# Kernel tuning notes

Hardware: AMD Instinct MI355X
Metric: run time of the kernel (lower is better)

The kernel has to match this reference:

```python
import jax, jax.numpy as jnp
import numpy as np

N = 100000
E = 1600000
DIN = 165
DH = 128


def setup_inputs() -> dict:
    key = jax.random.key(0)
    ks = jax.random.split(key, 10)
    def nrm(k, shape, scale=0.1):
        return jax.random.normal(k, shape, dtype=jnp.float32) * scale
    x = jax.random.normal(ks[0], (N, DIN), dtype=jnp.float32)
    edge_index = jax.random.randint(ks[1], (2, E), 0, N, dtype=jnp.int64)
    return dict(
        x=x,
        edge_index=edge_index,
        fb_w1=nrm(ks[2], (DIN, DIN // 2)),
        fb_w2=nrm(ks[3], (DIN // 2, DIN)),
        sage_wl=nrm(ks[4], (DIN, DH)),
        sage_bl=jnp.zeros((DH,), jnp.float32),
        sage_wr=nrm(ks[5], (DIN, DH)),
        gat_w=nrm(ks[6], (DH, DH // 2)),
        gat_att_src=nrm(ks[7], (DH // 2,)),
        gat_att_dst=nrm(ks[8], (DH // 2,)),
        gat_b=jnp.zeros((DH // 2,), jnp.float32),
        cheb_w=nrm(ks[9], (DH // 2, 1)),
        cheb_b=jnp.zeros((1,), jnp.float32),
    )


def _segment_softmax(logits, seg, num_segments):
    mx = jax.ops.segment_max(logits, seg, num_segments=num_segments)
    e = jnp.exp(logits - mx[seg])
    s = jax.ops.segment_sum(e, seg, num_segments=num_segments)
    return e / (s[seg] + 1e-16)


def reference(x, edge_index, fb_w1, fb_w2, sage_wl, sage_bl, sage_wr,
              gat_w, gat_att_src, gat_att_dst, gat_b, cheb_w, cheb_b):
    n = x.shape[0]
    src, dst = edge_index[0], edge_index[1]

    # FeatureBooster: scatter over batch=arange(n) is identity for max and sum,
    # so max_result == sum_result == x and y = sigmoid(mlp(x) + mlp(x)).
    m = jnp.maximum(x @ fb_w1, 0.0) @ fb_w2
    x = x * jax.nn.sigmoid(m + m)

    # SAGEConv (mean aggregation): out = lin_l(mean_agg(x_src -> dst)) + lin_r(x)
    agg = jax.ops.segment_sum(x[src], dst, num_segments=n)  # [n, DIN]
    cnt = jax.ops.segment_sum(jnp.ones((src.shape[0],), x.dtype), dst, num_segments=n)
    agg = agg / jnp.maximum(cnt, 1.0)[:, None]
    x = agg @ sage_wl + sage_bl + x @ sage_wr
    x = jnp.maximum(x, 0.0)  # relu; dropout is identity in eval mode

    # GATConv (heads=1) with default add_self_loops=True
    ar = jnp.arange(n, dtype=src.dtype)
    si = jnp.concatenate([src, ar])
    di = jnp.concatenate([dst, ar])
    h = x @ gat_w                      # [n, 64]
    a_s = h @ gat_att_src              # [n]
    a_d = h @ gat_att_dst              # [n]
    e = a_s[si] + a_d[di]
    e = jnp.where(e > 0, e, 0.2 * e)   # leaky_relu slope 0.2
    alpha = _segment_softmax(e, di, n)
    x = jax.ops.segment_sum(h[si] * alpha[:, None], di, num_segments=n) + gat_b
    x = jnp.maximum(x, 0.0)

    # ChebConv with K=1: T_0(x) = x, so it's a plain linear layer.
    x = x @ cheb_w + cheb_b
    return jax.nn.sigmoid(x)
```

## Files before the change

kernel.cpp:

```cpp
#include <hip/hip_runtime.h>
#include <hip/hip_bf16.h>

#define N_NODES 100000
#define N_EDGES 1600000
#define EQ 400000
#define DIN 165
#define DHID 82
#define DH 128
#define DG 64
#define XPS 168
#define HS 88
#define SLOTS 60
#define SCB 96

typedef _Float16 f16;
typedef f16 f16x8 __attribute__((ext_vector_type(8)));
typedef f16 f16x4 __attribute__((ext_vector_type(4)));
typedef float f32x4 __attribute__((ext_vector_type(4)));

#define MFMA16(a, b, c) __builtin_amdgcn_mfma_f32_16x16x32_f16(a, b, c, 0, 0, 0)


__device__ __forceinline__ void scatter_edges(int e0, int e1, int tg,
                                              const int* __restrict__ dst,
                                              const int* __restrict__ src,
                                              int* __restrict__ cnt,
                                              int* __restrict__ slots) {
    for (int e = e0 + tg; e < e1; e += SCB * 256) {
        int d = dst[e];
        int r = atomicAdd(&cnt[d], 1);
        if (r < SLOTS) slots[(long)d * SLOTS + r] = src[e];
    }
}

__global__ __launch_bounds__(256) void xpad_kernel(const float* __restrict__ x,
                                                   f16* __restrict__ Xp,
                                                   const int* __restrict__ dst,
                                                   const int* __restrict__ src,
                                                   int* __restrict__ cnt,
                                                   int* __restrict__ slots) {
    if (blockIdx.x < SCB) {
        scatter_edges(0, EQ, blockIdx.x * 256 + threadIdx.x, dst, src, cnt, slots);
        return;
    }
    int gid = (blockIdx.x - SCB) * 256 + threadIdx.x;
    if (gid >= N_NODES * 42) return;
    int node = gid / 42, g = gid % 42;
    int col0 = g * 4;
    f16x4 o;
#pragma unroll
    for (int j = 0; j < 4; j++) {
        int c = col0 + j;
        o[j] = (f16)((c < DIN) ? x[(long)node * DIN + c] : 0.f);
    }
    *((f16x4*)(Xp + (long)node * XPS + col0)) = o;
}

__global__ __launch_bounds__(256) void h_fill_kernel(const f16* __restrict__ Xp,
                                                     const float* __restrict__ w1,
                                                     f16* __restrict__ H,
                                                     const int* __restrict__ dst,
                                                     const int* __restrict__ src,
                                                     int* __restrict__ cnt,
                                                     int* __restrict__ slots) {
    int tid = threadIdx.x, wave = tid >> 6, lane = tid & 63;
    if (blockIdx.x < SCB) {
        scatter_edges(EQ, 2 * EQ, blockIdx.x * 256 + tid, dst, src, cnt, slots);
        return;
    }
    int q = lane >> 4, l16 = lane & 15;
    int blk = blockIdx.x - SCB;
    int g = (blk >> 3) & 1;
    int chunk = (blk & 7) + 8 * (blk >> 4);
    int nbase = g * 48;
    f16x8 bf[3][6];
#pragma unroll
    for (int nt = 0; nt < 3; nt++) {
        int col = nbase + nt * 16 + l16;
#pragma unroll
        for (int ks = 0; ks < 6; ks++) {
            int kb = ks * 32 + q * 8;
            f16x8 b;
#pragma unroll
            for (int j = 0; j < 8; j++) {
                int k = kb + j;
                b[j] = (f16)((k < DIN && col < DHID) ? w1[k * DHID + col] : 0.f);
            }
            bf[nt][ks] = b;
        }
    }
    for (int mt = chunk * 4 + wave; mt < 6250; mt += 768) {
        const f16* xr = Xp + (long)(mt * 16 + l16) * XPS;
        f32x4 acc[3];
#pragma unroll
        for (int nt = 0; nt < 3; nt++) acc[nt] = (f32x4){0.f, 0.f, 0.f, 0.f};
#pragma unroll
        for (int ks = 0; ks < 6; ks++) {
            f16x8 a = *((const f16x8*)(xr + ks * 32 + q * 8));
#pragma unroll
            for (int nt = 0; nt < 3; nt++) acc[nt] = MFMA16(a, bf[nt][ks], acc[nt]);
        }
#pragma unroll
        for (int nt = 0; nt < 3; nt++) {
            int col = nbase + nt * 16 + l16;
            if (col < HS) {
#pragma unroll
                for (int r = 0; r < 4; r++) {
                    int node = mt * 16 + q * 4 + r;
                    H[(long)node * HS + col] = (f16)fmaxf(acc[nt][r], 0.f);
                }
            }
        }
    }
}

__global__ __launch_bounds__(256) void y_kernel(const f16* __restrict__ Xp,
                                                const f16* __restrict__ H,
                                                const float* __restrict__ w2,
                                                f16* __restrict__ Y,
                                                const int* __restrict__ dst,
                                                const int* __restrict__ src,
                                                int* __restrict__ cnt,
                                                int* __restrict__ slots) {
    int tid = threadIdx.x, wave = tid >> 6, lane = tid & 63;
    if (blockIdx.x < SCB) {
        scatter_edges(2 * EQ, 3 * EQ, blockIdx.x * 256 + tid, dst, src, cnt, slots);
        return;
    }
    int q = lane >> 4, l16 = lane & 15;
    int blk = blockIdx.x - SCB;
    int g = (blk >> 3) & 3;
    int chunk = (blk & 7) + 8 * (blk >> 5);
    int nbase = g * 48;
    f16x8 bf[3][3];
#pragma unroll
    for (int nt = 0; nt < 3; nt++) {
        int col = nbase + nt * 16 + l16;
#pragma unroll
        for (int ks = 0; ks < 3; ks++) {
            int kb = ks * 32 + q * 8;
            f16x8 b;
#pragma unroll
            for (int j = 0; j < 8; j++) {
                int k = kb + j;
                b[j] = (f16)((k < DHID && col < DIN) ? w2[k * DIN + col] : 0.f);
            }
            bf[nt][ks] = b;
        }
    }
    for (int mt = chunk * 4 + wave; mt < 6250; mt += 768) {
        const f16* hr = H + (long)(mt * 16 + l16) * HS;
        f32x4 acc[3];
#pragma unroll
        for (int nt = 0; nt < 3; nt++) acc[nt] = (f32x4){0.f, 0.f, 0.f, 0.f};
#pragma unroll
        for (int ks = 0; ks < 3; ks++) {
            f16x8 a = *((const f16x8*)(hr + ks * 32 + q * 8));
#pragma unroll
            for (int nt = 0; nt < 3; nt++) acc[nt] = MFMA16(a, bf[nt][ks], acc[nt]);
        }
#pragma unroll
        for (int nt = 0; nt < 3; nt++) {
            int col = nbase + nt * 16 + l16;
            if (col < XPS) {
#pragma unroll
                for (int r = 0; r < 4; r++) {
                    int node = mt * 16 + q * 4 + r;
                    float gg = 1.f / (1.f + __expf(-2.f * acc[nt][r]));
                    float xv = (float)Xp[(long)node * XPS + col];
                    Y[(long)node * XPS + col] = (f16)(xv * gg);
                }
            }
        }
    }
}

__global__ __launch_bounds__(256) void sage_lin_kernel(const f16* __restrict__ Y,
                                                       const float* __restrict__ wl,
                                                       const float* __restrict__ wr,
                                                       const float* __restrict__ bl,
                                                       f16* __restrict__ t_l,
                                                       f16* __restrict__ x2,
                                                       const int* __restrict__ dst,
                                                       const int* __restrict__ src,
                                                       int* __restrict__ cnt,
                                                       int* __restrict__ slots) {
    int tid = threadIdx.x, wave = tid >> 6, lane = tid & 63;
    if (blockIdx.x < SCB) {
        scatter_edges(3 * EQ, N_EDGES, blockIdx.x * 256 + tid, dst, src, cnt, slots);
        return;
    }
    int q = lane >> 4, l16 = lane & 15;
    int blk = blockIdx.x - SCB;
    int g = (blk >> 3) & 3;
    int chunk = (blk & 7) + 8 * (blk >> 5);
    bool isR = (g >= 2);
    const float* W = isR ? wr : wl;
    int cbase = (g & 1) * 64;
    f16x8 bf[4][6];
    float blv[4];
#pragma unroll
    for (int nt = 0; nt < 4; nt++) {
        int col = cbase + nt * 16 + l16;
        blv[nt] = isR ? bl[col] : 0.f;
#pragma unroll
        for (int ks = 0; ks < 6; ks++) {
            int kb = ks * 32 + q * 8;
            f16x8 b;
#pragma unroll
            for (int j = 0; j < 8; j++) {
                int k = kb + j;
                b[j] = (f16)((k < DIN) ? W[k * DH + col] : 0.f);
            }
            bf[nt][ks] = b;
        }
    }
    for (int mt = chunk * 4 + wave; mt < 6250; mt += 768) {
        const f16* yrow = Y + (long)(mt * 16 + l16) * XPS;
        f32x4 acc[4];
#pragma unroll
        for (int nt = 0; nt < 4; nt++) acc[nt] = (f32x4){0.f, 0.f, 0.f, 0.f};
#pragma unroll
        for (int ks = 0; ks < 6; ks++) {
            f16x8 a = *((const f16x8*)(yrow + ks * 32 + q * 8));
#pragma unroll
            for (int nt = 0; nt < 4; nt++) acc[nt] = MFMA16(a, bf[nt][ks], acc[nt]);
        }
#pragma unroll
        for (int nt = 0; nt < 4; nt++) {
            int col = cbase + nt * 16 + l16;
#pragma unroll
            for (int r = 0; r < 4; r++) {
                int node = mt * 16 + q * 4 + r;
                if (isR)
                    x2[(long)node * DH + col] = (f16)(acc[nt][r] + blv[nt]);
                else
                    t_l[(long)node * DH + col] = (f16)acc[nt][r];
            }
        }
    }
}

__global__ __launch_bounds__(256) void sage_agg_kernel(const f16* __restrict__ t_l,
                                                       const int* __restrict__ cnt,
                                                       const int* __restrict__ slots,
                                                       f16* __restrict__ x2) {
    int wid = threadIdx.x >> 6, lane = threadIdx.x & 63;
    int i = blockIdx.x * 4 + wid;
    int deg = cnt[i];
    int quarter = lane >> 4, fq = lane & 15;
    float acc[8];
#pragma unroll
    for (int k = 0; k < 8; k++) acc[k] = 0.f;
    int sn_v = (lane < deg) ? slots[(long)i * SLOTS + lane] : 0;
    int jmax = (deg + 3) >> 2;
    for (int j = 0; j < jmax; j++) {
        int idx = 4 * j + quarter;
        int sn = __shfl(sn_v, idx);
        float v = (idx < deg) ? 1.f : 0.f;
        f16x8 p = *((const f16x8*)(t_l + ((long)sn << 7) + fq * 8));
#pragma unroll
        for (int k = 0; k < 8; k++) acc[k] = fmaf(v, (float)p[k], acc[k]);
    }
#pragma unroll
    for (int k = 0; k < 8; k++) {
        acc[k] += __shfl_xor(acc[k], 16);
        acc[k] += __shfl_xor(acc[k], 32);
    }
    if (quarter == 0) {
        float inv = 1.f / fmaxf((float)deg, 1.f);
        f16x8* xp = (f16x8*)(x2 + (long)i * DH + fq * 8);
        f16x8 pre = *xp;
        f16x8 o;
#pragma unroll
        for (int k = 0; k < 8; k++) o[k] = (f16)fmaxf((float)pre[k] + acc[k] * inv, 0.f);
        *xp = o;
    }
}

__global__ __launch_bounds__(256) void gat_h_kernel(const f16* __restrict__ x2,
                                                    const float* __restrict__ gw,
                                                    const float* __restrict__ att_s_w,
                                                    const float* __restrict__ att_d_w,
                                                    f16* __restrict__ h,
                                                    float* __restrict__ a_s,
                                                    float* __restrict__ a_d) {
    int tid = threadIdx.x, wave = tid >> 6, lane = tid & 63;
    int q = lane >> 4, l16 = lane & 15;
    f16x8 bf[4][4];
    float asw[4], adw[4];
#pragma unroll
    for (int nt = 0; nt < 4; nt++) {
        int col = nt * 16 + l16;
        asw[nt] = att_s_w[col];
        adw[nt] = att_d_w[col];
#pragma unroll
        for (int ks = 0; ks < 4; ks++) {
            int kb = ks * 32 + q * 8;
            f16x8 b;
#pragma unroll
            for (int j = 0; j < 8; j++) b[j] = (f16)gw[(kb + j) * DG + col];
            bf[nt][ks] = b;
        }
    }
    int stride = gridDim.x * 4;
    for (int mt = blockIdx.x * 4 + wave; mt < 6250; mt += stride) {
        const f16* xr = x2 + (long)(mt * 16 + l16) * DH;
        f32x4 acc[4];
#pragma unroll
        for (int nt = 0; nt < 4; nt++) acc[nt] = (f32x4){0.f, 0.f, 0.f, 0.f};
#pragma unroll
        for (int ks = 0; ks < 4; ks++) {
            f16x8 a = *((const f16x8*)(xr + ks * 32 + q * 8));
#pragma unroll
            for (int nt = 0; nt < 4; nt++) acc[nt] = MFMA16(a, bf[nt][ks], acc[nt]);
        }
#pragma unroll
        for (int r = 0; r < 4; r++) {
            int node = mt * 16 + q * 4 + r;
            float vs = 0.f, vd = 0.f;
#pragma unroll
            for (int nt = 0; nt < 4; nt++) {
                float hv = acc[nt][r];
                h[(long)node * DG + nt * 16 + l16] = (f16)hv;
                vs += hv * asw[nt];
                vd += hv * adw[nt];
            }
#pragma unroll
            for (int off = 1; off < 16; off <<= 1) {
                vs += __shfl_xor(vs, off);
                vd += __shfl_xor(vd, off);
            }
            if (l16 == 0) {
                a_s[node] = vs;
                a_d[node] = vd;
            }
        }
    }
}

__device__ __forceinline__ float leaky02(float v) { return v > 0.f ? v : 0.2f * v; }

__global__ __launch_bounds__(256) void gat_agg_kernel(const f16* __restrict__ h,
                                                      const float* __restrict__ a_s,
                                                      const float* __restrict__ a_d,
                                                      const int* __restrict__ cnt,
                                                      const int* __restrict__ slots,
                                                      const float* __restrict__ gat_b,
                                                      const float* __restrict__ cheb_w,
                                                      const float* __restrict__ cheb_b,
                                                      float* __restrict__ out) {
    int wid = threadIdx.x >> 6, lane = threadIdx.x & 63;
    int i = blockIdx.x * 4 + wid;
    int deg = cnt[i];
    int quarter = lane >> 4, fq = lane & 15;
    float adi = a_d[i];
    float acc[4] = {0.f, 0.f, 0.f, 0.f};
    int sn_v = (lane < deg) ? slots[(long)i * SLOTS + lane] : 0;
    float ev = 0.f;
    if (lane < deg) ev = __expf(leaky02(a_s[sn_v] + adi));
    float sv = ev;
    int jmax = (deg + 3) >> 2;
    for (int j = 0; j < jmax; j++) {
        int idx = 4 * j + quarter;
        int sn = __shfl(sn_v, idx);
        float w = __shfl(ev, idx);
        f16x4 p = *((const f16x4*)(h + ((long)sn << 6) + fq * 4));
#pragma unroll
        for (int k = 0; k < 4; k++) acc[k] = fmaf(w, (float)p[k], acc[k]);
    }
#pragma unroll
    for (int off = 32; off > 0; off >>= 1) sv += __shfl_xor(sv, off);
#pragma unroll
    for (int k = 0; k < 4; k++) {
        acc[k] += __shfl_xor(acc[k], 16);
        acc[k] += __shfl_xor(acc[k], 32);
    }
    if (quarter == 0) {
        float wself = __expf(leaky02(a_s[i] + adi));
        float s = sv + wself;
        f16x4 ph = *((const f16x4*)(h + ((long)i << 6) + fq * 4));
        float4 gb = ((const float4*)gat_b)[fq];
        float4 cw = ((const float4*)cheb_w)[fq];
        float gbv[4] = {gb.x, gb.y, gb.z, gb.w};
        float cwv[4] = {cw.x, cw.y, cw.z, cw.w};
        float inv = 1.f / s;
        float z = 0.f;
#pragma unroll
        for (int k = 0; k < 4; k++) {
            float o = fmaxf(fmaf(wself, (float)ph[k], acc[k]) * inv + gbv[k], 0.f);
            z = fmaf(o, cwv[k], z);
        }
#pragma unroll
        for (int off = 8; off > 0; off >>= 1) z += __shfl_xor(z, off);
        if (fq == 0) out[i] = 1.f / (1.f + __expf(-(z + cheb_b[0])));
    }
}

extern "C" void kernel_launch(void* const* d_in, const int* in_sizes, int n_in,
                              void* d_out, int out_size, void* d_ws, size_t ws_size,
                              hipStream_t stream) {
    const float* x       = (const float*)d_in[0];
    const int*   eidx    = (const int*)d_in[1];
    const float* fb_w1   = (const float*)d_in[2];
    const float* fb_w2   = (const float*)d_in[3];
    const float* sage_wl = (const float*)d_in[4];
    const float* sage_bl = (const float*)d_in[5];
    const float* sage_wr = (const float*)d_in[6];
    const float* gat_w   = (const float*)d_in[7];
    const float* att_src = (const float*)d_in[8];
    const float* att_dst = (const float*)d_in[9];
    const float* gat_b   = (const float*)d_in[10];
    const float* cheb_w  = (const float*)d_in[11];
    const float* cheb_b  = (const float*)d_in[12];

    const int* src = eidx;
    const int* dst = eidx + N_EDGES;

    char* base = (char*)d_ws;
    f16* Xp  = (f16*)base;
    f16* H   = (f16*)(base + 33600000);
    f16* Y   = (f16*)(base + 51200000);
    f16* t_l = (f16*)base;
    f16* x2  = (f16*)(base + 25600000);
    f16* h   = (f16*)(base + 51200000);
    float* a_s = (float*)(base + 64000000);
    float* a_d = a_s + N_NODES;
    int* cnt   = (int*)(base + 84800000);
    int* slots = (int*)(base + 85200000);

    hipMemsetAsync(cnt, 0, N_NODES * sizeof(int), stream);

    xpad_kernel<<<SCB + (N_NODES * 42 + 255) / 256, 256, 0, stream>>>(
        x, Xp, dst, src, cnt, slots);
    h_fill_kernel<<<SCB + 384, 256, 0, stream>>>(Xp, fb_w1, H, dst, src, cnt, slots);
    y_kernel<<<SCB + 768, 256, 0, stream>>>(Xp, H, fb_w2, Y, dst, src, cnt, slots);
    sage_lin_kernel<<<SCB + 768, 256, 0, stream>>>(Y, sage_wl, sage_wr, sage_bl,
                                                   t_l, x2, dst, src, cnt, slots);
    sage_agg_kernel<<<N_NODES / 4, 256, 0, stream>>>(t_l, cnt, slots, x2);
    gat_h_kernel<<<392, 256, 0, stream>>>(x2, gat_w, att_src, att_dst, h, a_s, a_d);
    gat_agg_kernel<<<N_NODES / 4, 256, 0, stream>>>(h, a_s, a_d, cnt, slots, gat_b,
                                                    cheb_w, cheb_b, (float*)d_out);
}
```

Before: 456.3 us.

## Fuse SAGE mean aggregation with GAT linear projection via shared-memory tile

Merges the SAGE neighbor aggregation kernel and the GAT h/attention projection kernel into one. Each block aggregates 16 nodes into a shared-memory tile, then runs MFMA on that tile to produce h, a_s and a_d, so the post-ReLU x2 no longer makes a global write-and-reload round trip. It also adds one kernel fewer and clamps the degree to SLOTS. In exchange, each block must reload the GAT weights from global memory and wait at a barrier between the gather and the MFMA phase, which may reduce latency hiding during the gather.

```diff
diff --git a/kernel.cpp b/kernel.cpp
--- a/kernel.cpp
+++ b/kernel.cpp
@@ -12,6 +12,7 @@
 #define HS 88
 #define SLOTS 60
 #define SCB 96
+#define TLP 136
 
 typedef _Float16 f16;
 typedef f16 f16x8 __attribute__((ext_vector_type(8)));
@@ -241,101 +242,96 @@
     }
 }
 
-__global__ __launch_bounds__(256) void sage_agg_kernel(const f16* __restrict__ t_l,
-                                                       const int* __restrict__ cnt,
-                                                       const int* __restrict__ slots,
-                                                       f16* __restrict__ x2) {
-    int wid = threadIdx.x >> 6, lane = threadIdx.x & 63;
-    int i = blockIdx.x * 4 + wid;
-    int deg = cnt[i];
+__global__ __launch_bounds__(256) void sage_agg_gat_kernel(const f16* __restrict__ t_l,
+                                                           const f16* __restrict__ x2pre,
+                                                           const int* __restrict__ cnt,
+                                                           const int* __restrict__ slots,
+                                                           const float* __restrict__ gw,
+                                                           const float* __restrict__ att_s_w,
+                                                           const float* __restrict__ att_d_w,
+                                                           f16* __restrict__ h,
+                                                           float* __restrict__ a_s,
+                                                           float* __restrict__ a_d) {
+    __shared__ f16 tile[16 * TLP];
+    __shared__ float ps[4][16], pd[4][16];
+    int tid = threadIdx.x, wid = tid >> 6, lane = tid & 63;
     int quarter = lane >> 4, fq = lane & 15;
-    float acc[8];
-#pragma unroll
-    for (int k = 0; k < 8; k++) acc[k] = 0.f;
-    int sn_v = (lane < deg) ? slots[(long)i * SLOTS + lane] : 0;
-    int jmax = (deg + 3) >> 2;
-    for (int j = 0; j < jmax; j++) {
-        int idx = 4 * j + quarter;
-        int sn = __shfl(sn_v, idx);
-        float v = (idx < deg) ? 1.f : 0.f;
-        f16x8 p = *((const f16x8*)(t_l + ((long)sn << 7) + fq * 8));
-#pragma unroll
-        for (int k = 0; k < 8; k++) acc[k] = fmaf(v, (float)p[k], acc[k]);
-    }
-#pragma unroll
-    for (int k = 0; k < 8; k++) {
-        acc[k] += __shfl_xor(acc[k], 16);
-        acc[k] += __shfl_xor(acc[k], 32);
-    }
-    if (quarter == 0) {
-        float inv = 1.f / fmaxf((float)deg, 1.f);
-        f16x8* xp = (f16x8*)(x2 + (long)i * DH + fq * 8);
-        f16x8 pre = *xp;
-        f16x8 o;
-#pragma unroll
-        for (int k = 0; k < 8; k++) o[k] = (f16)fmaxf((float)pre[k] + acc[k] * inv, 0.f);
-        *xp = o;
-    }
-}
-
-__global__ __launch_bounds__(256) void gat_h_kernel(const f16* __restrict__ x2,
-                                                    const float* __restrict__ gw,
-                                                    const float* __restrict__ att_s_w,
-                                                    const float* __restrict__ att_d_w,
-                                                    f16* __restrict__ h,
-                                                    float* __restrict__ a_s,
-                                                    float* __restrict__ a_d) {
-    int tid = threadIdx.x, wave = tid >> 6, lane = tid & 63;
-    int q = lane >> 4, l16 = lane & 15;
-    f16x8 bf[4][4];
-    float asw[4], adw[4];
-#pragma unroll
-    for (int nt = 0; nt < 4; nt++) {
-        int col = nt * 16 + l16;
-        asw[nt] = att_s_w[col];
-        adw[nt] = att_d_w[col];
-#pragma unroll
-        for (int ks = 0; ks < 4; ks++) {
-            int kb = ks * 32 + q * 8;
-            f16x8 b;
-#pragma unroll
-            for (int j = 0; j < 8; j++) b[j] = (f16)gw[(kb + j) * DG + col];
-            bf[nt][ks] = b;
-        }
-    }
-    int stride = gridDim.x * 4;
-    for (int mt = blockIdx.x * 4 + wave; mt < 6250; mt += stride) {
-        const f16* xr = x2 + (long)(mt * 16 + l16) * DH;
-        f32x4 acc[4];
-#pragma unroll
-        for (int nt = 0; nt < 4; nt++) acc[nt] = (f32x4){0.f, 0.f, 0.f, 0.f};
-#pragma unroll
-        for (int ks = 0; ks < 4; ks++) {
-            f16x8 a = *((const f16x8*)(xr + ks * 32 + q * 8));
-#pragma unroll
-            for (int nt = 0; nt < 4; nt++) acc[nt] = MFMA16(a, bf[nt][ks], acc[nt]);
-        }
-#pragma unroll
-        for (int r = 0; r < 4; r++) {
-            int node = mt * 16 + q * 4 + r;
-            float vs = 0.f, vd = 0.f;
-#pragma unroll
-            for (int nt = 0; nt < 4; nt++) {
-                float hv = acc[nt][r];
-                h[(long)node * DG + nt * 16 + l16] = (f16)hv;
-                vs += hv * asw[nt];
-                vd += hv * adw[nt];
-            }
-#pragma unroll
-            for (int off = 1; off < 16; off <<= 1) {
-                vs += __shfl_xor(vs, off);
-                vd += __shfl_xor(vd, off);
-            }
-            if (l16 == 0) {
-                a_s[node] = vs;
-                a_d[node] = vd;
-            }
-        }
+    int base = blockIdx.x * 16;
+
+    int q = quarter, l16 = fq;
+    f16x8 bf[4];
+#pragma unroll
+    for (int ks = 0; ks < 4; ks++) {
+        int kb = ks * 32 + q * 8;
+        f16x8 b;
+#pragma unroll
+        for (int j = 0; j < 8; j++) b[j] = (f16)gw[(kb + j) * DG + wid * 16 + l16];
+        bf[ks] = b;
+    }
+    float asw = att_s_w[wid * 16 + l16];
+    float adw = att_d_w[wid * 16 + l16];
+
+#pragma unroll
+    for (int s = 0; s < 4; s++) {
+        int row = wid * 4 + s;
+        int i = base + row;
+        int deg = min(cnt[i], SLOTS);
+        float acc[8];
+#pragma unroll
+        for (int k = 0; k < 8; k++) acc[k] = 0.f;
+        int sn_v = (lane < deg) ? slots[(long)i * SLOTS + lane] : 0;
+        int jmax = (deg + 3) >> 2;
+        for (int j = 0; j < jmax; j++) {
+            int idx = 4 * j + quarter;
+            int sn = __shfl(sn_v, idx);
+            float v = (idx < deg) ? 1.f : 0.f;
+            f16x8 p = *((const f16x8*)(t_l + ((long)sn << 7) + fq * 8));
+#pragma unroll
+            for (int k = 0; k < 8; k++) acc[k] = fmaf(v, (float)p[k], acc[k]);
+        }
+#pragma unroll
+        for (int k = 0; k < 8; k++) {
+            acc[k] += __shfl_xor(acc[k], 16);
+            acc[k] += __shfl_xor(acc[k], 32);
+        }
+        if (quarter == 0) {
+            float inv = 1.f / fmaxf((float)deg, 1.f);
+            f16x8 pre = *((const f16x8*)(x2pre + (long)i * DH + fq * 8));
+            f16x8 o;
+#pragma unroll
+            for (int k = 0; k < 8; k++)
+                o[k] = (f16)fmaxf((float)pre[k] + acc[k] * inv, 0.f);
+            *((f16x8*)(tile + row * TLP + fq * 8)) = o;
+        }
+    }
+    __syncthreads();
+
+    f32x4 acc2 = (f32x4){0.f, 0.f, 0.f, 0.f};
+#pragma unroll
+    for (int ks = 0; ks < 4; ks++) {
+        f16x8 a = *((const f16x8*)(tile + l16 * TLP + ks * 32 + q * 8));
+        acc2 = MFMA16(a, bf[ks], acc2);
+    }
+#pragma unroll
+    for (int r = 0; r < 4; r++) {
+        int m = q * 4 + r;
+        float hv = acc2[r];
+        h[(long)(base + m) * DG + wid * 16 + l16] = (f16)hv;
+        float vs = hv * asw, vd = hv * adw;
+#pragma unroll
+        for (int off = 1; off < 16; off <<= 1) {
+            vs += __shfl_xor(vs, off);
+            vd += __shfl_xor(vd, off);
+        }
+        if (l16 == 0) { ps[wid][m] = vs; pd[wid][m] = vd; }
+    }
+    __syncthreads();
+    if (wid == 0) {
+        int m = lane & 15, w = lane >> 4;
+        float vs = ps[w][m], vd = pd[w][m];
+        vs += __shfl_xor(vs, 16); vs += __shfl_xor(vs, 32);
+        vd += __shfl_xor(vd, 16); vd += __shfl_xor(vd, 32);
+        if (lane < 16) { a_s[base + m] = vs; a_d[base + m] = vd; }
     }
 }
 
@@ -352,7 +348,7 @@
                                                       float* __restrict__ out) {
     int wid = threadIdx.x >> 6, lane = threadIdx.x & 63;
     int i = blockIdx.x * 4 + wid;
-    int deg = cnt[i];
+    int deg = min(cnt[i], SLOTS);
     int quarter = lane >> 4, fq = lane & 15;
     float adi = a_d[i];
     float acc[4] = {0.f, 0.f, 0.f, 0.f};
@@ -422,7 +418,7 @@
     f16* H   = (f16*)(base + 33600000);
     f16* Y   = (f16*)(base + 51200000);
     f16* t_l = (f16*)base;
-    f16* x2  = (f16*)(base + 25600000);
+    f16* x2pre = (f16*)(base + 25600000);
     f16* h   = (f16*)(base + 51200000);
     float* a_s = (float*)(base + 64000000);
     float* a_d = a_s + N_NODES;
@@ -436,9 +432,9 @@
     h_fill_kernel<<<SCB + 384, 256, 0, stream>>>(Xp, fb_w1, H, dst, src, cnt, slots);
     y_kernel<<<SCB + 768, 256, 0, stream>>>(Xp, H, fb_w2, Y, dst, src, cnt, slots);
     sage_lin_kernel<<<SCB + 768, 256, 0, stream>>>(Y, sage_wl, sage_wr, sage_bl,
-                                                   t_l, x2, dst, src, cnt, slots);
-    sage_agg_kernel<<<N_NODES / 4, 256, 0, stream>>>(t_l, cnt, slots, x2);
-    gat_h_kernel<<<392, 256, 0, stream>>>(x2, gat_w, att_src, att_dst, h, a_s, a_d);
+                                                   t_l, x2pre, dst, src, cnt, slots);
+    sage_agg_gat_kernel<<<N_NODES / 16, 256, 0, stream>>>(
+        t_l, x2pre, cnt, slots, gat_w, att_src, att_dst, h, a_s, a_d);
     gat_agg_kernel<<<N_NODES / 4, 256, 0, stream>>>(h, a_s, a_d, cnt, slots, gat_b,
                                                     cheb_w, cheb_b, (float*)d_out);
 }
```

Result: slower. 468.9 us (+2.7%).
